# Performance work log

Hardware: AMD Instinct MI355X
Metric: run time of the kernel (lower is better)

## Reference

```python
import jax, jax.numpy as jnp
import numpy as np

KH, KW = 2, 2  # upsampling kernel size


def setup_inputs() -> dict:
    key = jax.random.key(0)
    k1, k2, k3 = jax.random.split(key, 3)
    x = jax.random.normal(k1, (4, 128, 128, 128), dtype=jnp.float32)
    # offset conv: Conv2d(C, 2*KH*KW, 3, padding=1). Torch zero-inits it; we use
    # small random weights so offsets are small (near-duplicate upsampling).
    w_off = jax.random.normal(k2, (2 * KH * KW, 128, 3, 3), dtype=jnp.float32) * 0.01
    b_off = jax.random.normal(k3, (2 * KH * KW,), dtype=jnp.float32) * 0.01
    return {"x": x, "w_off": w_off, "b_off": b_off}


def _bilinear_sample(x, sy, sx):
    """x: (N,C,H,W); sy,sx: (N,P,H,W) float sample coords. Zero outside bounds.
    Returns (N,P,C,H,W)."""
    N, C, H, W = x.shape
    P = sy.shape[1]
    xf = x.reshape(N, C, H * W)
    y0 = jnp.floor(sy)
    x0 = jnp.floor(sx)
    wy1 = sy - y0  # weight of lower (y0+1) row
    wx1 = sx - x0

    def gather(yi, xi):
        valid = (yi >= 0) & (yi <= H - 1) & (xi >= 0) & (xi <= W - 1)
        yc = jnp.clip(yi, 0, H - 1).astype(jnp.int32)
        xc = jnp.clip(xi, 0, W - 1).astype(jnp.int32)
        idx = (yc * W + xc).reshape(N, P, 1, H * W)
        idx_b = jnp.broadcast_to(idx, (N, P, C, H * W))
        xe = jnp.broadcast_to(xf[:, None], (N, P, C, H * W))
        v = jnp.take_along_axis(xe, idx_b, axis=-1).reshape(N, P, C, H, W)
        return v * valid.astype(x.dtype).reshape(N, P, 1, H, W)

    v00 = gather(y0, x0)
    v01 = gather(y0, x0 + 1)
    v10 = gather(y0 + 1, x0)
    v11 = gather(y0 + 1, x0 + 1)
    wy1e = wy1[:, :, None]  # (N,P,1,H,W)
    wx1e = wx1[:, :, None]
    return (v00 * (1 - wy1e) * (1 - wx1e)
            + v01 * (1 - wy1e) * wx1e
            + v10 * wy1e * (1 - wx1e)
            + v11 * wy1e * wx1e)


def reference(x, w_off, b_off):
    N, C, H, W = x.shape
    # offset = offset_conv(x): 3x3 conv, padding 1 -> (N, 2*KH*KW, H, W)
    off = jax.lax.conv_general_dilated(
        x, w_off, window_strides=(1, 1), padding='SAME',
        dimension_numbers=('NCHW', 'OIHW', 'NCHW')) + b_off[None, :, None, None]
    off = off.reshape(N, KH * KW, 2, H, W)  # per position p: (dy, dx)
    dy, dx = off[:, :, 0], off[:, :, 1]
    ys = jnp.arange(H, dtype=x.dtype)[None, None, :, None]
    xs = jnp.arange(W, dtype=x.dtype)[None, None, None, :]
    samp = _bilinear_sample(x, ys + dy, xs + dx)  # (N, KH*KW, C, H, W)
    # position p = i*KW + j -> output pixel (h*KH + i, w*KW + j)
    samp = samp.reshape(N, KH, KW, C, H, W).transpose(0, 3, 4, 1, 5, 2)
    return samp.reshape(N, C, H * KH, W * KW)
```

## Files before the change

### kernel.cpp

```cpp
#include <hip/hip_runtime.h>

#define H 128
#define W 128
#define C 128
#define NB 4
#define HW (H * W)
#define PXB 32
#define NSEG (W / PXB)
#define TPX 64

__global__ __launch_bounds__(256) void transpose_nchw_nhwc(
    const float* __restrict__ x, float* __restrict__ xt) {
  __shared__ float tile[TPX][C + 1];
  const int blk = blockIdx.x;
  const int n = blk >> 8;
  const int p0 = (blk & 255) * TPX;
  const float* xn = x + (size_t)n * C * HW;
  float* xtn = xt + (size_t)n * HW * C;

  const int i = threadIdx.x & 63;
  const int c0 = threadIdx.x >> 6;
#pragma unroll
  for (int c = c0; c < C; c += 4)
    tile[i][c] = xn[(size_t)c * HW + p0 + i];
  __syncthreads();

  const int cl = threadIdx.x & 31;
  const int pr = threadIdx.x >> 5;
#pragma unroll
  for (int p = pr; p < TPX; p += 8) {
    float4 v = make_float4(tile[p][4 * cl + 0], tile[p][4 * cl + 1],
                           tile[p][4 * cl + 2], tile[p][4 * cl + 3]);
    *(float4*)(xtn + (size_t)(p0 + p) * C + 4 * cl) = v;
  }
}

__global__ __launch_bounds__(256) void prep_wt(
    const float* __restrict__ wg, float* __restrict__ wt) {
  const int i = blockIdx.x * 256 + threadIdx.x;
  const int ch = i / 72;
  const int rem = i % 72;
  const int k = rem >> 3;
  const int p = rem & 7;
  wt[i] = wg[((size_t)p * C + ch) * 9 + k];
}

__global__ __launch_bounds__(256, 4) void dcn_fused_t3(
    const float* __restrict__ xt, const float* __restrict__ wt,
    const float* __restrict__ b, float* __restrict__ out) {

  __shared__ __align__(16) float lsh[4224];
  __shared__ float loff[PXB][9];
  __shared__ int4   ltapi[PXB][4];
  __shared__ float4 ltapw[PXB][4];

  const int t = threadIdx.x;
  const int bxr = blockIdx.x;
  const int bx = ((bxr & 7) << 8) | (bxr >> 3);
  const int seg = bx & (NSEG - 1);
  const int y = (bx >> 2) & (H - 1);
  const int n = bx >> 9;
  const int x0 = seg * PXB;

  const float* xtn = xt + (size_t)n * HW * C;

  {
    const int pp = t & 15;
    const int cg = t >> 4;
    const int xb = x0 + 2 * pp;
    const int cb = cg * 8;

    int xs[4];
    float colm[4];
#pragma unroll
    for (int j = 0; j < 4; ++j) {
      int xa = xb - 1 + j;
      colm[j] = ((unsigned)xa < (unsigned)W) ? 1.f : 0.f;
      xs[j] = xa < 0 ? 0 : (xa > W - 1 ? W - 1 : xa);
    }
    int pix[3][4];
    float m[3][4];
#pragma unroll
    for (int r = 0; r < 3; ++r) {
      int yy = y + r - 1;
      float rm = ((unsigned)yy < (unsigned)H) ? 1.f : 0.f;
      int yc = yy < 0 ? 0 : (yy > H - 1 ? H - 1 : yy);
#pragma unroll
      for (int j = 0; j < 4; ++j) {
        m[r][j] = rm * colm[j];
        pix[r][j] = yc * W + xs[j];
      }
    }

    float acc[2][8];
#pragma unroll
    for (int p = 0; p < 8; ++p) { acc[0][p] = 0.f; acc[1][p] = 0.f; }

#pragma unroll
    for (int c2 = 0; c2 < 2; ++c2) {
      float xvq[3][4][4];
#pragma unroll
      for (int r = 0; r < 3; ++r) {
#pragma unroll
        for (int j = 0; j < 4; ++j) {
          float4 v = *(const float4*)(xtn + (size_t)pix[r][j] * C + cb + c2 * 4);
          const float mm = m[r][j];
          xvq[r][j][0] = v.x * mm;
          xvq[r][j][1] = v.y * mm;
          xvq[r][j][2] = v.z * mm;
          xvq[r][j][3] = v.w * mm;
        }
      }
#pragma unroll
      for (int cc = 0; cc < 4; ++cc) {
        const int ch = cb + c2 * 4 + cc;
        const float4* wv4 = (const float4*)(wt + (size_t)ch * 72);
#pragma unroll
        for (int k = 0; k < 9; ++k) {
          const int r = k / 3, kw = k % 3;
          const float4 wa = wv4[2 * k];
          const float4 wb = wv4[2 * k + 1];
          const float xl = xvq[r][kw][cc];
          const float xr = xvq[r][kw + 1][cc];
          acc[0][0] += xl * wa.x; acc[0][1] += xl * wa.y;
          acc[0][2] += xl * wa.z; acc[0][3] += xl * wa.w;
          acc[0][4] += xl * wb.x; acc[0][5] += xl * wb.y;
          acc[0][6] += xl * wb.z; acc[0][7] += xl * wb.w;
          acc[1][0] += xr * wa.x; acc[1][1] += xr * wa.y;
          acc[1][2] += xr * wa.z; acc[1][3] += xr * wa.w;
          acc[1][4] += xr * wb.x; acc[1][5] += xr * wb.y;
          acc[1][6] += xr * wb.z; acc[1][7] += xr * wb.w;
        }
      }
    }
#pragma unroll
    for (int p = 0; p < 8; ++p) {
      lsh[((size_t)cg * PXB + 2 * pp) * 8 + p] = acc[0][p];
      lsh[((size_t)cg * PXB + 2 * pp + 1) * 8 + p] = acc[1][p];
    }
  }
  __syncthreads();

  {
    const int px = t >> 3;
    const int p = t & 7;
    float s = b[p];
#pragma unroll
    for (int g = 0; g < 16; ++g) s += lsh[((size_t)g * PXB + px) * 8 + p];
    loff[px][p] = s;
  }
  __syncthreads();

  if (t < 128) {
    const int px = t >> 2;
    const int pos = t & 3;
    const int xx = x0 + px;
    float sy = (float)y + loff[px][2 * pos];
    float sx = (float)xx + loff[px][2 * pos + 1];
    float y0f = floorf(sy), x0f = floorf(sx);
    float wy1 = sy - y0f, wx1 = sx - x0f;
    float wy0 = 1.f - wy1, wx0 = 1.f - wx1;
    int iy0 = (int)y0f, ix0 = (int)x0f;
    int iy1 = iy0 + 1, ix1 = ix0 + 1;
    float vy0 = ((unsigned)iy0 < (unsigned)H) ? 1.f : 0.f;
    float vy1 = ((unsigned)iy1 < (unsigned)H) ? 1.f : 0.f;
    float vx0 = ((unsigned)ix0 < (unsigned)W) ? 1.f : 0.f;
    float vx1 = ((unsigned)ix1 < (unsigned)W) ? 1.f : 0.f;
    int cy0 = iy0 < 0 ? 0 : (iy0 > H - 1 ? H - 1 : iy0);
    int cy1 = iy1 < 0 ? 0 : (iy1 > H - 1 ? H - 1 : iy1);
    int cx0 = ix0 < 0 ? 0 : (ix0 > W - 1 ? W - 1 : ix0);
    int cx1 = ix1 < 0 ? 0 : (ix1 > W - 1 ? W - 1 : ix1);
    ltapi[px][pos] = make_int4(cy0 * W + cx0, cy0 * W + cx1,
                               cy1 * W + cx0, cy1 * W + cx1);
    ltapw[px][pos] = make_float4(wy0 * wx0 * vy0 * vx0, wy0 * wx1 * vy0 * vx1,
                                 wy1 * wx0 * vy1 * vx0, wy1 * wx1 * vy1 * vx1);
  }
  __syncthreads();

  {
    const int cq = t & 31;
    const int pg = t >> 5;
    const int spx = t & 7;
    const int cg4 = t >> 3;
    const float4* xt4 = (const float4*)xtn;
    float4* lout4 = (float4*)lsh;
    float* outn = out + (size_t)n * C * (2 * H) * (2 * W);

    for (int pass = 0; pass < 4; ++pass) {
      const int px = pass * 8 + pg;
      float4 sacc[4];
#pragma unroll
      for (int pos = 0; pos < 4; ++pos) {
        const int4 o = ltapi[px][pos];
        const float4 wv = ltapw[px][pos];
        float4 v00 = xt4[(size_t)o.x * (C / 4) + cq];
        float4 v01 = xt4[(size_t)o.y * (C / 4) + cq];
        float4 v10 = xt4[(size_t)o.z * (C / 4) + cq];
        float4 v11 = xt4[(size_t)o.w * (C / 4) + cq];
        sacc[pos].x = wv.x * v00.x + wv.y * v01.x + wv.z * v10.x + wv.w * v11.x;
        sacc[pos].y = wv.x * v00.y + wv.y * v01.y + wv.z * v10.y + wv.w * v11.y;
        sacc[pos].z = wv.x * v00.z + wv.y * v01.z + wv.z * v10.z + wv.w * v11.z;
        sacc[pos].w = wv.x * v00.w + wv.y * v01.w + wv.z * v10.w + wv.w * v11.w;
      }
      __syncthreads();
#pragma unroll
      for (int pos = 0; pos < 4; ++pos)
        lout4[(pos * 8 + pg) * 33 + cq] = sacc[pos];
      __syncthreads();

      float4 v[4];
#pragma unroll
      for (int pos = 0; pos < 4; ++pos)
        v[pos] = lout4[(pos * 8 + spx) * 33 + cg4];
      const int xg = x0 + pass * 8 + spx;
      float* obase = outn + (size_t)(2 * y) * (2 * W) + 2 * xg;
#define STORE_CH(J, CMP)                                                      \
      {                                                                       \
        float* oc = obase + (size_t)(cg4 * 4 + J) * (4 * HW);                 \
        *(float2*)oc = make_float2(v[0].CMP, v[1].CMP);                       \
        *(float2*)(oc + 2 * W) = make_float2(v[2].CMP, v[3].CMP);             \
      }
      STORE_CH(0, x) STORE_CH(1, y) STORE_CH(2, z) STORE_CH(3, w)
#undef STORE_CH
    }
  }
}

__global__ __launch_bounds__(256) void dcn_fused(
    const float* __restrict__ x, const float* __restrict__ wg,
    const float* __restrict__ b, float* __restrict__ out) {

  __shared__ float lacc[16][PXB][8];
  __shared__ float loff[PXB][9];

  const int t = threadIdx.x;
  const int bx = blockIdx.x;
  const int seg = bx & (NSEG - 1);
  const int y = (bx >> 2) & (H - 1);
  const int n = bx >> 9;
  const int x0 = seg * PXB;

  const float* xn = x + (size_t)n * C * HW;

  {
    const int pp = t & 15;
    const int cg = t >> 4;
    const int xb = x0 + 2 * pp;

    int xs[4];
    float colm[4];
#pragma unroll
    for (int j = 0; j < 4; ++j) {
      int xa = xb - 1 + j;
      colm[j] = ((unsigned)xa < (unsigned)W) ? 1.f : 0.f;
      xs[j] = xa < 0 ? 0 : (xa > W - 1 ? W - 1 : xa);
    }
    int rowo[3];
    float m[3][4];
#pragma unroll
    for (int r = 0; r < 3; ++r) {
      int yy = y + r - 1;
      float rm = ((unsigned)yy < (unsigned)H) ? 1.f : 0.f;
      int yc = yy < 0 ? 0 : (yy > H - 1 ? H - 1 : yy);
      rowo[r] = yc * W;
#pragma unroll
      for (int j = 0; j < 4; ++j) m[r][j] = rm * colm[j];
    }

    float acc[2][8];
#pragma unroll
    for (int p = 0; p < 8; ++p) { acc[0][p] = 0.f; acc[1][p] = 0.f; }

    for (int c = 0; c < 8; ++c) {
      const int ch = cg * 8 + c;
      const float* xc = xn + (size_t)ch * HW;
      float xv[3][4];
#pragma unroll
      for (int r = 0; r < 3; ++r)
#pragma unroll
        for (int j = 0; j < 4; ++j)
          xv[r][j] = xc[rowo[r] + xs[j]] * m[r][j];

      const float* wc = wg + (size_t)ch * 9;
#pragma unroll
      for (int p = 0; p < 8; ++p) {
        const float* wp = wc + (size_t)p * C * 9;
#pragma unroll
        for (int r = 0; r < 3; ++r) {
#pragma unroll
          for (int kw = 0; kw < 3; ++kw) {
            const float wv = wp[r * 3 + kw];
            acc[0][p] += xv[r][kw] * wv;
            acc[1][p] += xv[r][kw + 1] * wv;
          }
        }
      }
    }
#pragma unroll
    for (int p = 0; p < 8; ++p) {
      lacc[cg][2 * pp][p] = acc[0][p];
      lacc[cg][2 * pp + 1][p] = acc[1][p];
    }
  }
  __syncthreads();

  {
    const int px = t >> 3;
    const int p = t & 7;
    float s = b[p];
#pragma unroll
    for (int g = 0; g < 16; ++g) s += lacc[g][px][p];
    loff[px][p] = s;
  }
  __syncthreads();

  {
    const int px = t & (PXB - 1);
    const int sg = t >> 5;
    const int xx = x0 + px;

    float offv[8];
#pragma unroll
    for (int q = 0; q < 8; ++q) offv[q] = loff[px][q];

    int o00[4], o01[4], o10[4], o11[4];
    float w00[4], w01[4], w10[4], w11[4];
#pragma unroll
    for (int p = 0; p < 4; ++p) {
      float sy = (float)y + offv[2 * p];
      float sx = (float)xx + offv[2 * p + 1];
      float y0f = floorf(sy), x0f = floorf(sx);
      float wy1 = sy - y0f, wx1 = sx - x0f;
      float wy0 = 1.f - wy1, wx0 = 1.f - wx1;
      int iy0 = (int)y0f, ix0 = (int)x0f;
      int iy1 = iy0 + 1, ix1 = ix0 + 1;
      float vy0 = ((unsigned)iy0 < (unsigned)H) ? 1.f : 0.f;
      float vy1 = ((unsigned)iy1 < (unsigned)H) ? 1.f : 0.f;
      float vx0 = ((unsigned)ix0 < (unsigned)W) ? 1.f : 0.f;
      float vx1 = ((unsigned)ix1 < (unsigned)W) ? 1.f : 0.f;
      int cy0 = iy0 < 0 ? 0 : (iy0 > H - 1 ? H - 1 : iy0);
      int cy1 = iy1 < 0 ? 0 : (iy1 > H - 1 ? H - 1 : iy1);
      int cx0 = ix0 < 0 ? 0 : (ix0 > W - 1 ? W - 1 : ix0);
      int cx1 = ix1 < 0 ? 0 : (ix1 > W - 1 ? W - 1 : ix1);
      o00[p] = cy0 * W + cx0; o01[p] = cy0 * W + cx1;
      o10[p] = cy1 * W + cx0; o11[p] = cy1 * W + cx1;
      w00[p] = wy0 * wx0 * vy0 * vx0;
      w01[p] = wy0 * wx1 * vy0 * vx1;
      w10[p] = wy1 * wx0 * vy1 * vx0;
      w11[p] = wy1 * wx1 * vy1 * vx1;
    }

    float* outn = out + (size_t)n * C * (2 * H) * (2 * W);
    for (int c = sg * 16; c < sg * 16 + 16; ++c) {
      const float* xc = xn + (size_t)c * HW;
      float s[4];
#pragma unroll
      for (int p = 0; p < 4; ++p) {
        s[p] = w00[p] * xc[o00[p]] + w01[p] * xc[o01[p]] +
               w10[p] * xc[o10[p]] + w11[p] * xc[o11[p]];
      }
      float* oc = outn + (size_t)c * (2 * H) * (2 * W);
      float2* r0 = (float2*)(oc + (size_t)(2 * y) * (2 * W) + 2 * xx);
      float2* r1 = (float2*)(oc + (size_t)(2 * y + 1) * (2 * W) + 2 * xx);
      *r0 = make_float2(s[0], s[1]);
      *r1 = make_float2(s[2], s[3]);
    }
  }
}

extern "C" void kernel_launch(void* const* d_in, const int* in_sizes, int n_in,
                              void* d_out, int out_size, void* d_ws, size_t ws_size,
                              hipStream_t stream) {
  const float* x = (const float*)d_in[0];
  const float* w = (const float*)d_in[1];
  const float* b = (const float*)d_in[2];
  float* out = (float*)d_out;

  const size_t xt_bytes = (size_t)NB * HW * C * sizeof(float);
  const size_t wt_bytes = (size_t)8 * C * 9 * sizeof(float);
  dim3 grid(NB * H * NSEG), block(256);

  if (d_ws != nullptr && ws_size >= xt_bytes + wt_bytes) {
    float* xt = (float*)d_ws;
    float* wt = (float*)((char*)d_ws + xt_bytes);
    prep_wt<<<dim3(36), block, 0, stream>>>(w, wt);
    transpose_nchw_nhwc<<<dim3(NB * (HW / TPX)), block, 0, stream>>>(x, xt);
    dcn_fused_t3<<<grid, block, 0, stream>>>(xt, wt, b, out);
  } else {
    dcn_fused<<<grid, block, 0, stream>>>(x, w, b, out);
  }
}
```

Baseline: 231.5 us.

## Stage conv weights in LDS, wave-shuffle reduce, and prefetch bilinear taps

The offset conv phase now stages conv weights into shared memory in two halves, so weights are no longer read per thread from global memory. The channel-group mapping is interleaved so partial sums can be reduced across lanes with shuffles before a small 4-way LDS reduction. The sampling loop is unrolled and software-pipelined, loading the next pass's four bilinear tap vectors while computing the current pass. This hides gather latency but raises register pressure under the 256x4 launch bound and adds extra syncs.

```diff
diff --git a/kernel.cpp b/kernel.cpp
--- a/kernel.cpp
+++ b/kernel.cpp
@@ -45,11 +45,12 @@
   wt[i] = wg[((size_t)p * C + ch) * 9 + k];
 }
 
-__global__ __launch_bounds__(256, 4) void dcn_fused_t3(
+__global__ __launch_bounds__(256, 4) void dcn_fused_t4(
     const float* __restrict__ xt, const float* __restrict__ wt,
     const float* __restrict__ b, float* __restrict__ out) {
 
-  __shared__ __align__(16) float lsh[4224];
+  __shared__ __align__(16) float lshu[64 * 76];
+  __shared__ float lacc2[4][PXB][9];
   __shared__ float loff[PXB][9];
   __shared__ int4   ltapi[PXB][4];
   __shared__ float4 ltapw[PXB][4];
@@ -68,7 +69,6 @@
     const int pp = t & 15;
     const int cg = t >> 4;
     const int xb = x0 + 2 * pp;
-    const int cb = cg * 8;
 
     int xs[4];
     float colm[4];
@@ -96,14 +96,29 @@
 #pragma unroll
     for (int p = 0; p < 8; ++p) { acc[0][p] = 0.f; acc[1][p] = 0.f; }
 
-#pragma unroll
-    for (int c2 = 0; c2 < 2; ++c2) {
+    const float4* wt4 = (const float4*)wt;
+
+#pragma unroll
+    for (int h = 0; h < 2; ++h) {
+      if (h) __syncthreads();
+#pragma unroll
+      for (int i = 0; i < 5; ++i) {
+        int idx = t + 256 * i;
+        if (idx < 1152) {
+          int chl = idx / 18;
+          int j = idx - chl * 18;
+          *(float4*)&lshu[chl * 76 + j * 4] = wt4[h * 1152 + idx];
+        }
+      }
+      __syncthreads();
+
+      const int cb4 = h * 16 + cg;
       float xvq[3][4][4];
 #pragma unroll
       for (int r = 0; r < 3; ++r) {
 #pragma unroll
         for (int j = 0; j < 4; ++j) {
-          float4 v = *(const float4*)(xtn + (size_t)pix[r][j] * C + cb + c2 * 4);
+          float4 v = *(const float4*)(xtn + (size_t)pix[r][j] * C + cb4 * 4);
           const float mm = m[r][j];
           xvq[r][j][0] = v.x * mm;
           xvq[r][j][1] = v.y * mm;
@@ -113,13 +128,13 @@
       }
 #pragma unroll
       for (int cc = 0; cc < 4; ++cc) {
-        const int ch = cb + c2 * 4 + cc;
-        const float4* wv4 = (const float4*)(wt + (size_t)ch * 72);
+        const int chl = cg * 4 + cc;
+        const float* wr = &lshu[chl * 76];
 #pragma unroll
         for (int k = 0; k < 9; ++k) {
           const int r = k / 3, kw = k % 3;
-          const float4 wa = wv4[2 * k];
-          const float4 wb = wv4[2 * k + 1];
+          const float4 wa = *(const float4*)&wr[k * 8];
+          const float4 wb = *(const float4*)&wr[k * 8 + 4];
           const float xl = xvq[r][kw][cc];
           const float xr = xvq[r][kw + 1][cc];
           acc[0][0] += xl * wa.x; acc[0][1] += xl * wa.y;
@@ -133,10 +148,22 @@
         }
       }
     }
-#pragma unroll
-    for (int p = 0; p < 8; ++p) {
-      lsh[((size_t)cg * PXB + 2 * pp) * 8 + p] = acc[0][p];
-      lsh[((size_t)cg * PXB + 2 * pp + 1) * 8 + p] = acc[1][p];
+
+#pragma unroll
+    for (int u = 0; u < 2; ++u) {
+#pragma unroll
+      for (int p = 0; p < 8; ++p) {
+        acc[u][p] += __shfl_xor(acc[u][p], 16);
+        acc[u][p] += __shfl_xor(acc[u][p], 32);
+      }
+    }
+    if ((t & 63) < 16) {
+      const int wv = t >> 6;
+#pragma unroll
+      for (int p = 0; p < 8; ++p) {
+        lacc2[wv][2 * pp][p] = acc[0][p];
+        lacc2[wv][2 * pp + 1][p] = acc[1][p];
+      }
     }
   }
   __syncthreads();
@@ -144,10 +171,8 @@
   {
     const int px = t >> 3;
     const int p = t & 7;
-    float s = b[p];
-#pragma unroll
-    for (int g = 0; g < 16; ++g) s += lsh[((size_t)g * PXB + px) * 8 + p];
-    loff[px][p] = s;
+    loff[px][p] = b[p] + lacc2[0][px][p] + lacc2[1][px][p] +
+                  lacc2[2][px][p] + lacc2[3][px][p];
   }
   __syncthreads();
 
@@ -183,24 +208,46 @@
     const int spx = t & 7;
     const int cg4 = t >> 3;
     const float4* xt4 = (const float4*)xtn;
-    float4* lout4 = (float4*)lsh;
+    float4* lout4 = (float4*)lshu;
     float* outn = out + (size_t)n * C * (2 * H) * (2 * W);
 
+    float4 wc_[4]; float4 nv_[16];
+#pragma unroll
+    for (int pos = 0; pos < 4; ++pos) {
+      const int4 o = ltapi[pg][pos];
+      wc_[pos] = ltapw[pg][pos];
+      nv_[4 * pos + 0] = xt4[(size_t)o.x * (C / 4) + cq];
+      nv_[4 * pos + 1] = xt4[(size_t)o.y * (C / 4) + cq];
+      nv_[4 * pos + 2] = xt4[(size_t)o.z * (C / 4) + cq];
+      nv_[4 * pos + 3] = xt4[(size_t)o.w * (C / 4) + cq];
+    }
+
+#pragma unroll
     for (int pass = 0; pass < 4; ++pass) {
-      const int px = pass * 8 + pg;
       float4 sacc[4];
 #pragma unroll
       for (int pos = 0; pos < 4; ++pos) {
-        const int4 o = ltapi[px][pos];
-        const float4 wv = ltapw[px][pos];
-        float4 v00 = xt4[(size_t)o.x * (C / 4) + cq];
-        float4 v01 = xt4[(size_t)o.y * (C / 4) + cq];
-        float4 v10 = xt4[(size_t)o.z * (C / 4) + cq];
-        float4 v11 = xt4[(size_t)o.w * (C / 4) + cq];
+        const float4 wv = wc_[pos];
+        const float4 v00 = nv_[4 * pos + 0];
+        const float4 v01 = nv_[4 * pos + 1];
+        const float4 v10 = nv_[4 * pos + 2];
+        const float4 v11 = nv_[4 * pos + 3];
         sacc[pos].x = wv.x * v00.x + wv.y * v01.x + wv.z * v10.x + wv.w * v11.x;
         sacc[pos].y = wv.x * v00.y + wv.y * v01.y + wv.z * v10.y + wv.w * v11.y;
         sacc[pos].z = wv.x * v00.z + wv.y * v01.z + wv.z * v10.z + wv.w * v11.z;
         sacc[pos].w = wv.x * v00.w + wv.y * v01.w + wv.z * v10.w + wv.w * v11.w;
+      }
+      if (pass < 3) {
+        const int pxn = (pass + 1) * 8 + pg;
+#pragma unroll
+        for (int pos = 0; pos < 4; ++pos) {
+          const int4 o = ltapi[pxn][pos];
+          wc_[pos] = ltapw[pxn][pos];
+          nv_[4 * pos + 0] = xt4[(size_t)o.x * (C / 4) + cq];
+          nv_[4 * pos + 1] = xt4[(size_t)o.y * (C / 4) + cq];
+          nv_[4 * pos + 2] = xt4[(size_t)o.z * (C / 4) + cq];
+          nv_[4 * pos + 3] = xt4[(size_t)o.w * (C / 4) + cq];
+        }
       }
       __syncthreads();
 #pragma unroll
@@ -385,7 +432,7 @@
     float* wt = (float*)((char*)d_ws + xt_bytes);
     prep_wt<<<dim3(36), block, 0, stream>>>(w, wt);
     transpose_nchw_nhwc<<<dim3(NB * (HW / TPX)), block, 0, stream>>>(x, xt);
-    dcn_fused_t3<<<grid, block, 0, stream>>>(xt, wt, b, out);
+    dcn_fused_t4<<<grid, block, 0, stream>>>(xt, wt, b, out);
   } else {
     dcn_fused<<<grid, block, 0, stream>>>(x, w, b, out);
   }
```

Measured after the change: 511.1 us. +120.8%, slower.

## Split fused deformable upsample into offset-table and sampling kernels

Applied to the files above, without the earlier changes.

Replaces the single fused conv+sampling kernel with two kernels: one computes the 3x3 offset conv and writes per-pixel bilinear index/weight tables to workspace, the other gathers NHWC features with those tables and writes the output with a layout suited to coalesced stores. This unfuses the stages to reduce register/LDS pressure and give each phase its own thread mapping. In exchange it adds an extra launch plus about 4 MB of table traffic, and it needs a larger workspace. If the workspace is too small, it falls back to the old fused path.

```diff
diff --git a/kernel.cpp b/kernel.cpp
--- a/kernel.cpp
+++ b/kernel.cpp
@@ -43,6 +43,183 @@
   const int k = rem >> 3;
   const int p = rem & 7;
   wt[i] = wg[((size_t)p * C + ch) * 9 + k];
+}
+
+__global__ __launch_bounds__(256, 4) void dcn_offsets(
+    const float* __restrict__ xt, const float* __restrict__ wt,
+    const float* __restrict__ b, int4* __restrict__ tabi,
+    float4* __restrict__ tabw) {
+
+  __shared__ __align__(16) float lsh[4096];
+  __shared__ float loff[PXB][9];
+
+  const int t = threadIdx.x;
+  const int bxr = blockIdx.x;
+  const int bx = ((bxr & 7) << 8) | (bxr >> 3);
+  const int seg = bx & (NSEG - 1);
+  const int y = (bx >> 2) & (H - 1);
+  const int n = bx >> 9;
+  const int x0 = seg * PXB;
+
+  const float* xtn = xt + (size_t)n * HW * C;
+
+  {
+    const int pp = t & 15;
+    const int cg = t >> 4;
+    const int xb = x0 + 2 * pp;
+    const int cb = cg * 8;
+
+    int xs[4];
+    float colm[4];
+#pragma unroll
+    for (int j = 0; j < 4; ++j) {
+      int xa = xb - 1 + j;
+      colm[j] = ((unsigned)xa < (unsigned)W) ? 1.f : 0.f;
+      xs[j] = xa < 0 ? 0 : (xa > W - 1 ? W - 1 : xa);
+    }
+    int pix[3][4];
+    float m[3][4];
+#pragma unroll
+    for (int r = 0; r < 3; ++r) {
+      int yy = y + r - 1;
+      float rm = ((unsigned)yy < (unsigned)H) ? 1.f : 0.f;
+      int yc = yy < 0 ? 0 : (yy > H - 1 ? H - 1 : yy);
+#pragma unroll
+      for (int j = 0; j < 4; ++j) {
+        m[r][j] = rm * colm[j];
+        pix[r][j] = yc * W + xs[j];
+      }
+    }
+
+    float acc[2][8];
+#pragma unroll
+    for (int p = 0; p < 8; ++p) { acc[0][p] = 0.f; acc[1][p] = 0.f; }
+
+#pragma unroll
+    for (int c2 = 0; c2 < 2; ++c2) {
+      float xvq[3][4][4];
+#pragma unroll
+      for (int r = 0; r < 3; ++r) {
+#pragma unroll
+        for (int j = 0; j < 4; ++j) {
+          float4 v = *(const float4*)(xtn + (size_t)pix[r][j] * C + cb + c2 * 4);
+          const float mm = m[r][j];
+          xvq[r][j][0] = v.x * mm;
+          xvq[r][j][1] = v.y * mm;
+          xvq[r][j][2] = v.z * mm;
+          xvq[r][j][3] = v.w * mm;
+        }
+      }
+#pragma unroll
+      for (int cc = 0; cc < 4; ++cc) {
+        const int ch = cb + c2 * 4 + cc;
+        const float4* wv4 = (const float4*)(wt + (size_t)ch * 72);
+#pragma unroll
+        for (int k = 0; k < 9; ++k) {
+          const int r = k / 3, kw = k % 3;
+          const float4 wa = wv4[2 * k];
+          const float4 wb = wv4[2 * k + 1];
+          const float xl = xvq[r][kw][cc];
+          const float xr = xvq[r][kw + 1][cc];
+          acc[0][0] += xl * wa.x; acc[0][1] += xl * wa.y;
+          acc[0][2] += xl * wa.z; acc[0][3] += xl * wa.w;
+          acc[0][4] += xl * wb.x; acc[0][5] += xl * wb.y;
+          acc[0][6] += xl * wb.z; acc[0][7] += xl * wb.w;
+          acc[1][0] += xr * wa.x; acc[1][1] += xr * wa.y;
+          acc[1][2] += xr * wa.z; acc[1][3] += xr * wa.w;
+          acc[1][4] += xr * wb.x; acc[1][5] += xr * wb.y;
+          acc[1][6] += xr * wb.z; acc[1][7] += xr * wb.w;
+        }
+      }
+    }
+#pragma unroll
+    for (int p = 0; p < 8; ++p) {
+      lsh[((size_t)cg * PXB + 2 * pp) * 8 + p] = acc[0][p];
+      lsh[((size_t)cg * PXB + 2 * pp + 1) * 8 + p] = acc[1][p];
+    }
+  }
+  __syncthreads();
+
+  {
+    const int px = t >> 3;
+    const int p = t & 7;
+    float s = b[p];
+#pragma unroll
+    for (int g = 0; g < 16; ++g) s += lsh[((size_t)g * PXB + px) * 8 + p];
+    loff[px][p] = s;
+  }
+  __syncthreads();
+
+  if (t < 128) {
+    const int px = t >> 2;
+    const int pos = t & 3;
+    const int xx = x0 + px;
+    float sy = (float)y + loff[px][2 * pos];
+    float sx = (float)xx + loff[px][2 * pos + 1];
+    float y0f = floorf(sy), x0f = floorf(sx);
+    float wy1 = sy - y0f, wx1 = sx - x0f;
+    float wy0 = 1.f - wy1, wx0 = 1.f - wx1;
+    int iy0 = (int)y0f, ix0 = (int)x0f;
+    int iy1 = iy0 + 1, ix1 = ix0 + 1;
+    float vy0 = ((unsigned)iy0 < (unsigned)H) ? 1.f : 0.f;
+    float vy1 = ((unsigned)iy1 < (unsigned)H) ? 1.f : 0.f;
+    float vx0 = ((unsigned)ix0 < (unsigned)W) ? 1.f : 0.f;
+    float vx1 = ((unsigned)ix1 < (unsigned)W) ? 1.f : 0.f;
+    int cy0 = iy0 < 0 ? 0 : (iy0 > H - 1 ? H - 1 : iy0);
+    int cy1 = iy1 < 0 ? 0 : (iy1 > H - 1 ? H - 1 : iy1);
+    int cx0 = ix0 < 0 ? 0 : (ix0 > W - 1 ? W - 1 : ix0);
+    int cx1 = ix1 < 0 ? 0 : (ix1 > W - 1 ? W - 1 : ix1);
+    const size_t gp = ((size_t)(n * H + y) * W + xx) * 4 + pos;
+    tabi[gp] = make_int4((cy0 * W + cx0) * (C / 4), (cy0 * W + cx1) * (C / 4),
+                         (cy1 * W + cx0) * (C / 4), (cy1 * W + cx1) * (C / 4));
+    tabw[gp] = make_float4(wy0 * wx0 * vy0 * vx0, wy0 * wx1 * vy0 * vx1,
+                           wy1 * wx0 * vy1 * vx0, wy1 * wx1 * vy1 * vx1);
+  }
+}
+
+__global__ __launch_bounds__(256, 4) void dcn_sample(
+    const float* __restrict__ xt, const int4* __restrict__ tabi,
+    const float4* __restrict__ tabw, float* __restrict__ out) {
+  const int braw = blockIdx.x;
+  const int bk = ((braw & 7) << 10) | (braw >> 3);
+  const int t = threadIdx.x;
+  const int seg8 = bk & 15;
+  const int y = (bk >> 4) & (H - 1);
+  const int n = bk >> 11;
+  const int pair2 = t & 3;
+  const int q = (t >> 2) & 31;
+  const int half = t >> 7;
+
+  const float4* xt4n = (const float4*)xt + (size_t)n * HW * (C / 4);
+  const size_t rowb = (size_t)(n * H + y) * W;
+
+  float sc[2][2][4];
+#pragma unroll
+  for (int bb = 0; bb < 2; ++bb) {
+#pragma unroll
+    for (int pp2 = 0; pp2 < 2; ++pp2) {
+      const int px = seg8 * 8 + 2 * pair2 + bb;
+      const size_t gp = (rowb + px) * 4 + 2 * half + pp2;
+      const int4 o = tabi[gp];
+      const float4 wv = tabw[gp];
+      const float4 v00 = xt4n[o.x + q];
+      const float4 v01 = xt4n[o.y + q];
+      const float4 v10 = xt4n[o.z + q];
+      const float4 v11 = xt4n[o.w + q];
+      sc[bb][pp2][0] = wv.x * v00.x + wv.y * v01.x + wv.z * v10.x + wv.w * v11.x;
+      sc[bb][pp2][1] = wv.x * v00.y + wv.y * v01.y + wv.z * v10.y + wv.w * v11.y;
+      sc[bb][pp2][2] = wv.x * v00.z + wv.y * v01.z + wv.z * v10.z + wv.w * v11.z;
+      sc[bb][pp2][3] = wv.x * v00.w + wv.y * v01.w + wv.z * v10.w + wv.w * v11.w;
+    }
+  }
+
+  float* obase = out + (size_t)n * C * 4 * HW +
+                 (size_t)(2 * y + half) * (2 * W) + 16 * seg8 + 4 * pair2;
+#pragma unroll
+  for (int j = 0; j < 4; ++j) {
+    *(float4*)(obase + (size_t)(4 * q + j) * (4 * HW)) =
+        make_float4(sc[0][0][j], sc[0][1][j], sc[1][0][j], sc[1][1][j]);
+  }
 }
 
 __global__ __launch_bounds__(256, 4) void dcn_fused_t3(
@@ -378,15 +555,27 @@
 
   const size_t xt_bytes = (size_t)NB * HW * C * sizeof(float);
   const size_t wt_bytes = (size_t)8 * C * 9 * sizeof(float);
-  dim3 grid(NB * H * NSEG), block(256);
-
-  if (d_ws != nullptr && ws_size >= xt_bytes + wt_bytes) {
+  const size_t tab_cnt = (size_t)NB * HW * 4;
+  const size_t tabi_bytes = tab_cnt * sizeof(int4);
+  const size_t tabw_bytes = tab_cnt * sizeof(float4);
+  dim3 block(256);
+
+  if (d_ws != nullptr && ws_size >= xt_bytes + wt_bytes + tabi_bytes + tabw_bytes) {
+    float* xt = (float*)d_ws;
+    float* wt = (float*)((char*)d_ws + xt_bytes);
+    int4* tabi = (int4*)((char*)d_ws + xt_bytes + wt_bytes);
+    float4* tabw = (float4*)((char*)d_ws + xt_bytes + wt_bytes + tabi_bytes);
+    prep_wt<<<dim3(36), block, 0, stream>>>(w, wt);
+    transpose_nchw_nhwc<<<dim3(NB * (HW / TPX)), block, 0, stream>>>(x, xt);
+    dcn_offsets<<<dim3(NB * H * NSEG), block, 0, stream>>>(xt, wt, b, tabi, tabw);
+    dcn_sample<<<dim3(NB * H * 16), block, 0, stream>>>(xt, tabi, tabw, out);
+  } else if (d_ws != nullptr && ws_size >= xt_bytes + wt_bytes) {
     float* xt = (float*)d_ws;
     float* wt = (float*)((char*)d_ws + xt_bytes);
     prep_wt<<<dim3(36), block, 0, stream>>>(w, wt);
     transpose_nchw_nhwc<<<dim3(NB * (HW / TPX)), block, 0, stream>>>(x, xt);
-    dcn_fused_t3<<<grid, block, 0, stream>>>(xt, wt, b, out);
+    dcn_fused_t3<<<dim3(NB * H * NSEG), block, 0, stream>>>(xt, wt, b, out);
   } else {
-    dcn_fused<<<grid, block, 0, stream>>>(x, w, b, out);
-  }
-}
+    dcn_fused<<<dim3(NB * H * NSEG), block, 0, stream>>>(x, w, b, out);
+  }
+}
```

After: 294.7 us. +27.3%, slower.

## Stage bilinear tap window in LDS and restructure output stores

Applied to the files above, without the earlier changes.

Each block now computes the bounding box of all bilinear tap positions using wave shuffles and a small LDS reduction. It copies that window of NHWC input (up to 120 pixels × 128 channels) into shared memory and serves the taps from LDS, falling back to global memory for taps outside the window. The output phase is remapped so each thread writes float4 rows directly, removing the LDS transpose and its two barriers per pass. The LDS footprint grows to about 63 KB, so launch bounds drop to 2 blocks per CU, which may reduce occupancy and latency hiding.

```diff
diff --git a/kernel.cpp b/kernel.cpp
--- a/kernel.cpp
+++ b/kernel.cpp
@@ -8,6 +8,9 @@
 #define PXB 32
 #define NSEG (W / PXB)
 #define TPX 64
+#define SPX 120
+#define CMAX 40
+#define PSTR 132
 
 __global__ __launch_bounds__(256) void transpose_nchw_nhwc(
     const float* __restrict__ x, float* __restrict__ xt) {
@@ -45,14 +48,16 @@
   wt[i] = wg[((size_t)p * C + ch) * 9 + k];
 }
 
-__global__ __launch_bounds__(256, 4) void dcn_fused_t3(
+__global__ __launch_bounds__(256, 2) void dcn_fused_t6(
     const float* __restrict__ xt, const float* __restrict__ wt,
     const float* __restrict__ b, float* __restrict__ out) {
 
-  __shared__ __align__(16) float lsh[4224];
+  __shared__ __align__(16) float lstage[SPX * PSTR];
   __shared__ float loff[PXB][9];
   __shared__ int4   ltapi[PXB][4];
   __shared__ float4 ltapw[PXB][4];
+  __shared__ int lred[4][4];
+  __shared__ int lwin[4];
 
   const int t = threadIdx.x;
   const int bxr = blockIdx.x;
@@ -135,8 +140,8 @@
     }
 #pragma unroll
     for (int p = 0; p < 8; ++p) {
-      lsh[((size_t)cg * PXB + 2 * pp) * 8 + p] = acc[0][p];
-      lsh[((size_t)cg * PXB + 2 * pp + 1) * 8 + p] = acc[1][p];
+      lstage[((size_t)cg * PXB + 2 * pp) * 8 + p] = acc[0][p];
+      lstage[((size_t)cg * PXB + 2 * pp + 1) * 8 + p] = acc[1][p];
     }
   }
   __syncthreads();
@@ -146,82 +151,124 @@
     const int p = t & 7;
     float s = b[p];
 #pragma unroll
-    for (int g = 0; g < 16; ++g) s += lsh[((size_t)g * PXB + px) * 8 + p];
+    for (int g = 0; g < 16; ++g) s += lstage[((size_t)g * PXB + px) * 8 + p];
     loff[px][p] = s;
   }
   __syncthreads();
 
-  if (t < 128) {
-    const int px = t >> 2;
-    const int pos = t & 3;
-    const int xx = x0 + px;
-    float sy = (float)y + loff[px][2 * pos];
-    float sx = (float)xx + loff[px][2 * pos + 1];
-    float y0f = floorf(sy), x0f = floorf(sx);
-    float wy1 = sy - y0f, wx1 = sx - x0f;
-    float wy0 = 1.f - wy1, wx0 = 1.f - wx1;
-    int iy0 = (int)y0f, ix0 = (int)x0f;
-    int iy1 = iy0 + 1, ix1 = ix0 + 1;
-    float vy0 = ((unsigned)iy0 < (unsigned)H) ? 1.f : 0.f;
-    float vy1 = ((unsigned)iy1 < (unsigned)H) ? 1.f : 0.f;
-    float vx0 = ((unsigned)ix0 < (unsigned)W) ? 1.f : 0.f;
-    float vx1 = ((unsigned)ix1 < (unsigned)W) ? 1.f : 0.f;
-    int cy0 = iy0 < 0 ? 0 : (iy0 > H - 1 ? H - 1 : iy0);
-    int cy1 = iy1 < 0 ? 0 : (iy1 > H - 1 ? H - 1 : iy1);
-    int cx0 = ix0 < 0 ? 0 : (ix0 > W - 1 ? W - 1 : ix0);
-    int cx1 = ix1 < 0 ? 0 : (ix1 > W - 1 ? W - 1 : ix1);
-    ltapi[px][pos] = make_int4(cy0 * W + cx0, cy0 * W + cx1,
-                               cy1 * W + cx0, cy1 * W + cx1);
-    ltapw[px][pos] = make_float4(wy0 * wx0 * vy0 * vx0, wy0 * wx1 * vy0 * vx1,
-                                 wy1 * wx0 * vy1 * vx0, wy1 * wx1 * vy1 * vx1);
-  }
-  __syncthreads();
-
-  {
-    const int cq = t & 31;
-    const int pg = t >> 5;
-    const int spx = t & 7;
-    const int cg4 = t >> 3;
-    const float4* xt4 = (const float4*)xtn;
-    float4* lout4 = (float4*)lsh;
-    float* outn = out + (size_t)n * C * (2 * H) * (2 * W);
-
+  {
+    int ymin = H, ymax = 0, xmin = W, xmax = 0;
+    if (t < 128) {
+      const int px = t >> 2;
+      const int pos = t & 3;
+      const int xx = x0 + px;
+      float sy = (float)y + loff[px][2 * pos];
+      float sx = (float)xx + loff[px][2 * pos + 1];
+      float y0f = floorf(sy), x0f = floorf(sx);
+      float wy1 = sy - y0f, wx1 = sx - x0f;
+      float wy0 = 1.f - wy1, wx0 = 1.f - wx1;
+      int iy0 = (int)y0f, ix0 = (int)x0f;
+      int iy1 = iy0 + 1, ix1 = ix0 + 1;
+      float vy0 = ((unsigned)iy0 < (unsigned)H) ? 1.f : 0.f;
+      float vy1 = ((unsigned)iy1 < (unsigned)H) ? 1.f : 0.f;
+      float vx0 = ((unsigned)ix0 < (unsigned)W) ? 1.f : 0.f;
+      float vx1 = ((unsigned)ix1 < (unsigned)W) ? 1.f : 0.f;
+      int cy0 = iy0 < 0 ? 0 : (iy0 > H - 1 ? H - 1 : iy0);
+      int cy1 = iy1 < 0 ? 0 : (iy1 > H - 1 ? H - 1 : iy1);
+      int cx0 = ix0 < 0 ? 0 : (ix0 > W - 1 ? W - 1 : ix0);
+      int cx1 = ix1 < 0 ? 0 : (ix1 > W - 1 ? W - 1 : ix1);
+      ltapi[px][pos] = make_int4(cy0 * W + cx0, cy0 * W + cx1,
+                                 cy1 * W + cx0, cy1 * W + cx1);
+      ltapw[px][pos] = make_float4(wy0 * wx0 * vy0 * vx0, wy0 * wx1 * vy0 * vx1,
+                                   wy1 * wx0 * vy1 * vx0, wy1 * wx1 * vy1 * vx1);
+      ymin = cy0; ymax = cy1; xmin = cx0 < cx1 ? cx0 : cx1;
+      xmax = cx0 > cx1 ? cx0 : cx1;
+    }
+#pragma unroll
+    for (int d = 1; d < 64; d <<= 1) {
+      int v;
+      v = __shfl_xor(ymin, d); ymin = v < ymin ? v : ymin;
+      v = __shfl_xor(ymax, d); ymax = v > ymax ? v : ymax;
+      v = __shfl_xor(xmin, d); xmin = v < xmin ? v : xmin;
+      v = __shfl_xor(xmax, d); xmax = v > xmax ? v : xmax;
+    }
+    if ((t & 63) == 0) {
+      const int wv = t >> 6;
+      lred[wv][0] = ymin; lred[wv][1] = ymax;
+      lred[wv][2] = xmin; lred[wv][3] = xmax;
+    }
+    __syncthreads();
+    if (t == 0) {
+      int py0 = lred[0][0] < lred[1][0] ? lred[0][0] : lred[1][0];
+      int py1 = lred[0][1] > lred[1][1] ? lred[0][1] : lred[1][1];
+      int qx0 = lred[0][2] < lred[1][2] ? lred[0][2] : lred[1][2];
+      int qx1 = lred[0][3] > lred[1][3] ? lred[0][3] : lred[1][3];
+      int cols = qx1 - qx0 + 1;
+      if (cols > CMAX) cols = CMAX;
+      int rows = py1 - py0 + 1;
+      int rmax = SPX / cols;
+      if (rows > rmax) rows = rmax;
+      lwin[0] = py0; lwin[1] = qx0; lwin[2] = rows; lwin[3] = cols;
+    }
+    __syncthreads();
+  }
+
+  const int py0 = lwin[0], qx0 = lwin[1], Rr = lwin[2], Cc = lwin[3];
+  const float4* xt4 = (const float4*)xtn;
+  {
+    const int nf = Cc * 32;
+#pragma unroll 1
+    for (int r = 0; r < Rr; ++r) {
+      const float4* src = xt4 + (size_t)((py0 + r) * W + qx0) * 32;
+      for (int i = t; i < nf; i += 256) {
+        const int c = i >> 5, quad = i & 31;
+        *(float4*)&lstage[(r * Cc + c) * PSTR + 4 * quad] = src[i];
+      }
+    }
+  }
+  __syncthreads();
+
+  {
+    const int pair = t & 3;
+    const int q = (t >> 2) & 31;
+    const int half = t >> 7;
+    float* outn = out + (size_t)n * C * 4 * HW;
+
+#pragma unroll 1
     for (int pass = 0; pass < 4; ++pass) {
-      const int px = pass * 8 + pg;
-      float4 sacc[4];
-#pragma unroll
-      for (int pos = 0; pos < 4; ++pos) {
-        const int4 o = ltapi[px][pos];
-        const float4 wv = ltapw[px][pos];
-        float4 v00 = xt4[(size_t)o.x * (C / 4) + cq];
-        float4 v01 = xt4[(size_t)o.y * (C / 4) + cq];
-        float4 v10 = xt4[(size_t)o.z * (C / 4) + cq];
-        float4 v11 = xt4[(size_t)o.w * (C / 4) + cq];
-        sacc[pos].x = wv.x * v00.x + wv.y * v01.x + wv.z * v10.x + wv.w * v11.x;
-        sacc[pos].y = wv.x * v00.y + wv.y * v01.y + wv.z * v10.y + wv.w * v11.y;
-        sacc[pos].z = wv.x * v00.z + wv.y * v01.z + wv.z * v10.z + wv.w * v11.z;
-        sacc[pos].w = wv.x * v00.w + wv.y * v01.w + wv.z * v10.w + wv.w * v11.w;
-      }
-      __syncthreads();
-#pragma unroll
-      for (int pos = 0; pos < 4; ++pos)
-        lout4[(pos * 8 + pg) * 33 + cq] = sacc[pos];
-      __syncthreads();
-
-      float4 v[4];
-#pragma unroll
-      for (int pos = 0; pos < 4; ++pos)
-        v[pos] = lout4[(pos * 8 + spx) * 33 + cg4];
-      const int xg = x0 + pass * 8 + spx;
-      float* obase = outn + (size_t)(2 * y) * (2 * W) + 2 * xg;
-#define STORE_CH(J, CMP)                                                      \
-      {                                                                       \
-        float* oc = obase + (size_t)(cg4 * 4 + J) * (4 * HW);                 \
-        *(float2*)oc = make_float2(v[0].CMP, v[1].CMP);                       \
-        *(float2*)(oc + 2 * W) = make_float2(v[2].CMP, v[3].CMP);             \
-      }
-      STORE_CH(0, x) STORE_CH(1, y) STORE_CH(2, z) STORE_CH(3, w)
-#undef STORE_CH
+      const int px0p = pass * 8 + 2 * pair;
+      float sc[2][2][4];
+#pragma unroll
+      for (int bb = 0; bb < 2; ++bb) {
+#pragma unroll
+        for (int pp2 = 0; pp2 < 2; ++pp2) {
+          const int pos = 2 * half + pp2;
+          const int4 o = ltapi[px0p + bb][pos];
+          const float4 wv = ltapw[px0p + bb][pos];
+          float4 tv[4];
+          const int oo[4] = {o.x, o.y, o.z, o.w};
+#pragma unroll
+          for (int j = 0; j < 4; ++j) {
+            const int idx = oo[j];
+            const int rr = (idx >> 7) - py0;
+            const int cc2 = (idx & 127) - qx0;
+            if ((unsigned)rr < (unsigned)Rr && (unsigned)cc2 < (unsigned)Cc)
+              tv[j] = *(const float4*)&lstage[(rr * Cc + cc2) * PSTR + 4 * q];
+            else
+              tv[j] = xt4[(size_t)idx * 32 + q];
+          }
+          sc[bb][pp2][0] = wv.x * tv[0].x + wv.y * tv[1].x + wv.z * tv[2].x + wv.w * tv[3].x;
+          sc[bb][pp2][1] = wv.x * tv[0].y + wv.y * tv[1].y + wv.z * tv[2].y + wv.w * tv[3].y;
+          sc[bb][pp2][2] = wv.x * tv[0].z + wv.y * tv[1].z + wv.z * tv[2].z + wv.w * tv[3].z;
+          sc[bb][pp2][3] = wv.x * tv[0].w + wv.y * tv[1].w + wv.z * tv[2].w + wv.w * tv[3].w;
+        }
+      }
+      float* obase = outn + (size_t)(2 * y + half) * (2 * W) + 2 * (x0 + px0p);
+#pragma unroll
+      for (int j = 0; j < 4; ++j) {
+        *(float4*)(obase + (size_t)(4 * q + j) * (4 * HW)) =
+            make_float4(sc[0][0][j], sc[0][1][j], sc[1][0][j], sc[1][1][j]);
+      }
     }
   }
 }
@@ -378,15 +425,15 @@
 
   const size_t xt_bytes = (size_t)NB * HW * C * sizeof(float);
   const size_t wt_bytes = (size_t)8 * C * 9 * sizeof(float);
-  dim3 grid(NB * H * NSEG), block(256);
+  dim3 block(256);
 
   if (d_ws != nullptr && ws_size >= xt_bytes + wt_bytes) {
     float* xt = (float*)d_ws;
     float* wt = (float*)((char*)d_ws + xt_bytes);
     prep_wt<<<dim3(36), block, 0, stream>>>(w, wt);
     transpose_nchw_nhwc<<<dim3(NB * (HW / TPX)), block, 0, stream>>>(x, xt);
-    dcn_fused_t3<<<grid, block, 0, stream>>>(xt, wt, b, out);
+    dcn_fused_t6<<<dim3(NB * H * NSEG), block, 0, stream>>>(xt, wt, b, out);
   } else {
-    dcn_fused<<<grid, block, 0, stream>>>(x, w, b, out);
+    dcn_fused<<<dim3(NB * H * NSEG), block, 0, stream>>>(x, w, b, out);
   }
 }
```

Result: slower. 248.1 us (+7.2%).
